# Kernel tuning notes

Hardware: AMD Instinct MI355X
Metric: run time of the kernel (lower is better)

## Reference

```python
import jax, jax.numpy as jnp
import numpy as np

V = 50000      # word vocab
CV = 128       # char vocab
E = 64         # char embedding size
H = 512        # GRU hidden / word embedding size
T = 20         # max spelling length
B = 2048       # batch of words


def setup_inputs() -> dict:
    key = jax.random.key(0)
    ks = jax.random.split(key, 8)
    chars = jax.random.randint(ks[0], (V, T), 1, CV)
    lengths = jax.random.randint(ks[1], (V,), 1, T + 1)
    mask = jnp.arange(T)[None, :] < lengths[:, None]
    chars = jnp.where(mask, chars, 0)  # padding_idx = 0 beyond each length
    spelling_table = jnp.concatenate([chars, lengths[:, None]], axis=1).astype(jnp.int32)
    data = jax.random.randint(ks[2], (B,), 0, V).astype(jnp.int32)
    s = 1.0 / np.sqrt(H)
    emb = (jax.random.normal(ks[3], (CV, E), jnp.float32) * 0.1).at[0].set(0.0)
    W_ih = jax.random.uniform(ks[4], (3 * H, E), jnp.float32, -s, s)
    W_hh = jax.random.uniform(ks[5], (3 * H, H), jnp.float32, -s, s)
    b_ih = jax.random.uniform(ks[6], (3 * H,), jnp.float32, -s, s)
    b_hh = jax.random.uniform(ks[7], (3 * H,), jnp.float32, -s, s)
    return {"data": data, "spelling_table": spelling_table, "emb": emb,
            "W_ih": W_ih, "W_hh": W_hh, "b_ih": b_ih, "b_hh": b_hh}


def reference(data, spelling_table, emb, W_ih, W_hh, b_ih, b_hh):
    H_ = W_hh.shape[1]
    rec = spelling_table[data]            # [B, T+1] gather of spellings
    spelling = rec[:, :-1]                # [B, T] char ids
    lengths = rec[:, -1]                  # [B]
    # torch.sort(lengths, descending=True): stable descending argsort
    perm = jnp.argsort(-lengths)
    sorted_sp = spelling[perm]            # [B, T]
    sorted_len = lengths[perm]            # [B]
    x = emb[sorted_sp]                    # [B, T, E]
    # precompute input projections for all timesteps (fused r|z|n gates)
    xW = jnp.einsum('bte,ge->btg', x, W_ih) + b_ih   # [B, T, 3H]
    valid = (jnp.arange(x.shape[1])[None, :] < sorted_len[:, None])  # [B, T]

    def step(h, inp):
        xw_t, v_t = inp                   # [B, 3H], [B, 1]
        hW = h @ W_hh.T + b_hh            # [B, 3H]
        xr, xz, xn = jnp.split(xw_t, 3, axis=-1)
        hr, hz, hn = jnp.split(hW, 3, axis=-1)
        r = jax.nn.sigmoid(xr + hr)
        z = jax.nn.sigmoid(xz + hz)
        n = jnp.tanh(xn + r * hn)
        h_new = (1.0 - z) * n + z * h
        h = jnp.where(v_t, h_new, h)      # packed-sequence semantics
        return h, None

    h0 = jnp.zeros((x.shape[0], H_), x.dtype)
    ht, _ = jax.lax.scan(step, h0, (jnp.swapaxes(xW, 0, 1), valid.T[:, :, None]))
    # faithful reproduction of the original's unsort: ht[sorted_length_idx]
    return ht[perm]
```

## Files before the change

kernel.cpp:

```cpp
#include <hip/hip_runtime.h>
#include <hip/hip_bf16.h>
#include <math.h>

#define B_  2048
#define E_  64
#define H_  512
#define T_  20

typedef _Float16 half8 __attribute__((ext_vector_type(8)));
typedef __attribute__((ext_vector_type(4))) float f32x4;
typedef unsigned long long u64;

#define mf16(a, b, c) __builtin_amdgcn_mfma_f32_16x16x32_f16(a, b, c, 0, 0, 0)

__device__ __forceinline__ float sigmoidf_(float x) {
  return 1.0f / (1.0f + __expf(-x));
}
__device__ __forceinline__ float tanh_fast(float x) {
  float e = __expf(2.0f * x);
  return 1.0f - 2.0f / (e + 1.0f);
}

__global__ __launch_bounds__(256) void k_setup(const int* __restrict__ data,
                                               const int* __restrict__ st,
                                               int* __restrict__ perm,
                                               int* __restrict__ iperm,
                                               int* __restrict__ Mt,
                                               int* __restrict__ bar) {
  __shared__ int lens[B_];
  __shared__ int hist[256][22];
  __shared__ int sub[16][22];
  __shared__ int subpre[16][22];
  __shared__ int cnt[32];
  __shared__ int offs[32];
  int tid = threadIdx.x;

  #pragma unroll
  for (int i = 0; i < 4; ++i) bar[tid * 4 + i] = 0;

  #pragma unroll
  for (int q = 0; q < 8; ++q) {
    int i = tid * 8 + q;
    lens[i] = st[data[i] * (T_ + 1) + T_];
  }
  #pragma unroll
  for (int L = 0; L < 22; ++L) hist[tid][L] = 0;
  #pragma unroll
  for (int q = 0; q < 8; ++q) hist[tid][lens[tid * 8 + q]]++;
  __syncthreads();

  for (int q = tid; q < 16 * 21; q += 256) {
    int g = q / 21, L = q % 21;
    int run = 0;
    for (int j = 0; j < 16; ++j) {
      int v = hist[g * 16 + j][L];
      hist[g * 16 + j][L] = run;
      run += v;
    }
    sub[g][L] = run;
  }
  __syncthreads();
  if (tid < 21) {
    int run = 0;
    for (int g = 0; g < 16; ++g) { subpre[g][tid] = run; run += sub[g][tid]; }
    cnt[tid] = run;
  }
  __syncthreads();
  if (tid <= 20) {
    int s = 0;
    for (int L = tid + 1; L <= 20; ++L) s += cnt[L];
    offs[tid] = s;
  }
  __syncthreads();
  if (tid < T_) Mt[tid] = offs[tid];

  int g = tid >> 4;
  #pragma unroll
  for (int q = 0; q < 8; ++q) {
    int i = tid * 8 + q;
    int L = lens[i];
    int rk = subpre[g][L] + hist[tid][L];
    hist[tid][L] += 1;
    perm[offs[L] + rk] = i;
  }
  __syncthreads();
  #pragma unroll
  for (int q = 0; q < 8; ++q) {
    int i = tid * 8 + q;
    iperm[perm[i]] = i;
  }
}

__global__ void k_schars(const int* __restrict__ data, const int* __restrict__ st,
                         const int* __restrict__ perm, int* __restrict__ schars_T) {
  int idx = blockIdx.x * 256 + threadIdx.x;
  if (idx >= B_ * T_) return;
  int t = idx >> 11;
  int j = idx & (B_ - 1);
  schars_T[idx] = st[data[perm[j]] * (T_ + 1) + t];
}

__global__ void k_wconv(const float* __restrict__ W_ih, const float* __restrict__ W_hh,
                        _Float16* __restrict__ Wp) {
  int idx = blockIdx.x * 256 + threadIdx.x;
  if (idx >= 8 * 18 * 12 * 512) return;
  int e = idx & 7;
  int l = (idx >> 3) & 63;
  int rest = idx >> 9;
  int g = rest % 3;  rest /= 3;
  int w = rest & 3;  rest >>= 2;
  int c = rest % 18;
  int cb = rest / 18;
  int grow = g * H_ + cb * 64 + w * 16 + (l & 15);
  int k = c * 32 + (l >> 4) * 8 + e;
  float v = (k < E_) ? W_ih[grow * E_ + k] : W_hh[grow * H_ + (k - E_)];
  Wp[idx] = (_Float16)v;
}

__global__ void k_embconv(const float* __restrict__ emb, _Float16* __restrict__ embp) {
  int idx = blockIdx.x * 256 + threadIdx.x;
  if (idx >= 128 * E_) return;
  embp[idx] = (_Float16)emb[idx];
}

__global__ __launch_bounds__(256, 1) void k_gru(
    const int* __restrict__ Mt, const int* __restrict__ schars_T,
    const _Float16* __restrict__ embp, const _Float16* __restrict__ Wp,
    const float* __restrict__ b_ih, const float* __restrict__ b_hh,
    _Float16* __restrict__ hq0, _Float16* __restrict__ hq1,
    const int* __restrict__ iperm, float* __restrict__ out,
    int* __restrict__ bar) {
  __shared__ __attribute__((aligned(16))) _Float16 As[64][512];
  __shared__ __attribute__((aligned(16))) _Float16 Hs[64][68];

  int bid = blockIdx.x;
  int rb = bid & 31, cb = bid >> 5;
  int m0 = rb * 64;
  int tid = threadIdx.x;
  int w = tid >> 6;
  int l = tid & 63;
  int ln = l & 15, kc = l >> 4;

  half8 wfr[54];
  const _Float16* wsrc = Wp + ((size_t)(cb * 18) * 12 + w * 3) * 512 + l * 8;
  #pragma unroll
  for (int c = 0; c < 18; ++c) {
    #pragma unroll
    for (int g = 0; g < 3; ++g)
      wfr[c * 3 + g] = *(const half8*)(wsrc + (c * 12 + g) * 512);
  }

  int colg = cb * 64 + w * 16 + ln;
  float br  = b_ih[colg] + b_hh[colg];
  float bz  = b_ih[H_ + colg] + b_hh[H_ + colg];
  float bnx = b_ih[2 * H_ + colg];
  float bnh = b_hh[2 * H_ + colg];

  float hreg[4][4];
  #pragma unroll
  for (int i = 0; i < 4; ++i)
    #pragma unroll
    for (int j = 0; j < 4; ++j) hreg[i][j] = 0.0f;

  int* barp = bar + rb * 32;

  for (int t = 0; t < T_; ++t) {
    int M = Mt[t];
    if (m0 >= M) break;
    const _Float16* hin = (t & 1) ? hq1 : hq0;
    _Float16*       hout = (t & 1) ? hq0 : hq1;

    int ch[4];
    #pragma unroll
    for (int rf = 0; rf < 4; ++rf)
      ch[rf] = schars_T[t * B_ + m0 + rf * 16 + ln];

    u64 sb[16][2];
    if (t > 0) {
      if (tid == 0) {
        int target = 8 * t;
        while (__hip_atomic_load(barp, __ATOMIC_RELAXED, __HIP_MEMORY_SCOPE_AGENT) < target) {}
      }
      __syncthreads();
      #pragma unroll
      for (int i = 0; i < 16; ++i) {
        int r = w * 16 + i;
        u64* src = (u64*)(hin + (size_t)(m0 + r) * H_) + ((l ^ (i & 7)) << 1);
        sb[i][0] = __hip_atomic_load(src, __ATOMIC_RELAXED, __HIP_MEMORY_SCOPE_AGENT);
        sb[i][1] = __hip_atomic_load(src + 1, __ATOMIC_RELAXED, __HIP_MEMORY_SCOPE_AGENT);
      }
    }

    f32x4 accr[4], accz[4], accnx[4], accnh[4];
    #pragma unroll
    for (int i = 0; i < 4; ++i) {
      accr[i] = (f32x4){0.f, 0.f, 0.f, 0.f};
      accz[i] = (f32x4){0.f, 0.f, 0.f, 0.f};
      accnx[i] = (f32x4){0.f, 0.f, 0.f, 0.f};
      accnh[i] = (f32x4){0.f, 0.f, 0.f, 0.f};
    }

    #pragma unroll
    for (int rf = 0; rf < 4; ++rf) {
      const _Float16* ep = embp + ch[rf] * E_ + kc * 8;
      half8 a0 = *(const half8*)ep;
      half8 a1 = *(const half8*)(ep + 32);
      accr[rf]  = mf16(a0, wfr[0], accr[rf]);
      accz[rf]  = mf16(a0, wfr[1], accz[rf]);
      accnx[rf] = mf16(a0, wfr[2], accnx[rf]);
      accr[rf]  = mf16(a1, wfr[3], accr[rf]);
      accz[rf]  = mf16(a1, wfr[4], accz[rf]);
      accnx[rf] = mf16(a1, wfr[5], accnx[rf]);
    }

    if (t > 0) {
      #pragma unroll
      for (int i = 0; i < 16; ++i) {
        int r = w * 16 + i;
        u64* dp = (u64*)&As[r][l * 8];
        dp[0] = sb[i][0];
        dp[1] = sb[i][1];
      }
    }
    __syncthreads();

    if (t > 0) {
      const _Float16* asb = &As[0][0];
      #pragma unroll
      for (int chk = 0; chk < 16; ++chk) {
        #pragma unroll
        for (int rf = 0; rf < 4; ++rf) {
          int r = rf * 16 + ln;
          half8 af = *(const half8*)(asb + r * 512 + (((chk * 4 + kc) ^ (ln & 7)) << 3));
          accr[rf]  = mf16(af, wfr[(chk + 2) * 3 + 0], accr[rf]);
          accz[rf]  = mf16(af, wfr[(chk + 2) * 3 + 1], accz[rf]);
          accnh[rf] = mf16(af, wfr[(chk + 2) * 3 + 2], accnh[rf]);
        }
      }
    }

    #pragma unroll
    for (int rf = 0; rf < 4; ++rf) {
      #pragma unroll
      for (int q = 0; q < 4; ++q) {
        int row_l = rf * 16 + kc * 4 + q;
        if (m0 + row_l < M) {
          float r_ = sigmoidf_(accr[rf][q] + br);
          float z_ = sigmoidf_(accz[rf][q] + bz);
          float n_ = tanh_fast(accnx[rf][q] + bnx + r_ * (accnh[rf][q] + bnh));
          float hnew = (1.0f - z_) * n_ + z_ * hreg[rf][q];
          hreg[rf][q] = hnew;
          Hs[row_l][w * 16 + ln] = (_Float16)hnew;
        }
      }
    }
    __syncthreads();

    #pragma unroll
    for (int j = 0; j < 4; ++j) {
      int c = tid + 256 * j;
      int row_l = c >> 4;
      int coff = (c & 15) * 4;
      if (m0 + row_l < M) {
        u64 v = *(const u64*)&Hs[row_l][coff];
        __hip_atomic_store((u64*)(hout + (size_t)(m0 + row_l) * H_ + cb * 64 + coff),
                           v, __ATOMIC_RELAXED, __HIP_MEMORY_SCOPE_AGENT);
      }
    }
    asm volatile("s_waitcnt vmcnt(0)" ::: "memory");
    __syncthreads();
    if (tid == 0) {
      __hip_atomic_fetch_add(barp, 1, __ATOMIC_RELAXED, __HIP_MEMORY_SCOPE_AGENT);
    }
  }

  #pragma unroll
  for (int rf = 0; rf < 4; ++rf) {
    #pragma unroll
    for (int q = 0; q < 4; ++q) {
      int row = m0 + rf * 16 + kc * 4 + q;
      out[(size_t)iperm[row] * H_ + colg] = hreg[rf][q];
    }
  }
}

extern "C" void kernel_launch(void* const* d_in, const int* in_sizes, int n_in,
                              void* d_out, int out_size, void* d_ws, size_t ws_size,
                              hipStream_t stream) {
  const int*   data = (const int*)d_in[0];
  const int*   st   = (const int*)d_in[1];
  const float* emb  = (const float*)d_in[2];
  const float* W_ih = (const float*)d_in[3];
  const float* W_hh = (const float*)d_in[4];
  const float* b_ih = (const float*)d_in[5];
  const float* b_hh = (const float*)d_in[6];
  float* out = (float*)d_out;

  _Float16* hq0  = (_Float16*)d_ws;
  _Float16* hq1  = hq0 + B_ * H_;
  _Float16* Wp   = hq1 + B_ * H_;
  _Float16* embp = Wp + 8 * 18 * 12 * 512;
  int* perm   = (int*)(embp + 128 * E_);
  int* iperm  = perm + B_;
  int* Mt     = iperm + B_;
  int* bar    = Mt + 32;
  int* schars = bar + 32 * 32;

  k_setup<<<1, 256, 0, stream>>>(data, st, perm, iperm, Mt, bar);
  k_schars<<<(B_ * T_ + 255) / 256, 256, 0, stream>>>(data, st, perm, schars);
  k_wconv<<<(8 * 18 * 12 * 512 + 255) / 256, 256, 0, stream>>>(W_ih, W_hh, Wp);
  k_embconv<<<(128 * E_ + 255) / 256, 256, 0, stream>>>(emb, embp);

  k_gru<<<dim3(256), dim3(256), 0, stream>>>(Mt, schars, embp, Wp, b_ih, b_hh,
                                             hq0, hq1, iperm, out, bar);
}
```

Baseline: 188.7 us.

## Replace row-group counter barrier with per-block flags and overlap own-slice MFMA

Each block now publishes a per-block step flag instead of incrementing a shared row-group counter. It also keeps its own hidden-state slice in shared memory and runs that slice's MFMAs before waiting on peers. Peer slices are then fetched and consumed chunk by chunk with a rotated order, so recurrence work overlaps the cross-block synchronisation and global loads. This adds all-thread polling of seven flags and more __syncthreads per step, and it relies on relaxed atomics for correctness.

```diff
diff --git a/kernel.cpp b/kernel.cpp
--- a/kernel.cpp
+++ b/kernel.cpp
@@ -73,6 +73,7 @@
   }
   __syncthreads();
   if (tid < T_) Mt[tid] = offs[tid];
+  if (tid >= T_ && tid < 32) Mt[tid] = 0;
 
   int g = tid >> 4;
   #pragma unroll
@@ -129,26 +130,36 @@
     const float* __restrict__ b_ih, const float* __restrict__ b_hh,
     _Float16* __restrict__ hq0, _Float16* __restrict__ hq1,
     const int* __restrict__ iperm, float* __restrict__ out,
-    int* __restrict__ bar) {
+    int* __restrict__ flags) {
   __shared__ __attribute__((aligned(16))) _Float16 As[64][512];
-  __shared__ __attribute__((aligned(16))) _Float16 Hs[64][68];
 
   int bid = blockIdx.x;
   int rb = bid & 31, cb = bid >> 5;
   int m0 = rb * 64;
   int tid = threadIdx.x;
-  int w = tid >> 6;
-  int l = tid & 63;
+  int w = tid >> 6, l = tid & 63;
   int ln = l & 15, kc = l >> 4;
+  int rS = tid >> 2, qS = tid & 3;
 
   half8 wfr[54];
-  const _Float16* wsrc = Wp + ((size_t)(cb * 18) * 12 + w * 3) * 512 + l * 8;
-  #pragma unroll
-  for (int c = 0; c < 18; ++c) {
-    #pragma unroll
-    for (int g = 0; g < 3; ++g)
-      wfr[c * 3 + g] = *(const half8*)(wsrc + (c * 12 + g) * 512);
-  }
+#define WLD(c, g) (*(const half8*)(Wp + ((((size_t)cb * 18 + (c)) * 4 + w) * 3 + (g)) * 512 + l * 8))
+  #pragma unroll
+  for (int g = 0; g < 3; ++g) {
+    wfr[0 + g] = WLD(0, g);
+    wfr[3 + g] = WLD(1, g);
+    wfr[6 + g] = WLD(2 + 2 * cb, g);
+    wfr[9 + g] = WLD(3 + 2 * cb, g);
+  }
+  #pragma unroll
+  for (int jj = 0; jj < 7; ++jj) {
+    int j = (cb + 1 + jj) & 7;
+    #pragma unroll
+    for (int c2 = 0; c2 < 2; ++c2)
+      #pragma unroll
+      for (int g = 0; g < 3; ++g)
+        wfr[12 + jj * 6 + c2 * 3 + g] = WLD(2 + 2 * j + c2, g);
+  }
+#undef WLD
 
   int colg = cb * 64 + w * 16 + ln;
   float br  = b_ih[colg] + b_hh[colg];
@@ -162,34 +173,21 @@
     #pragma unroll
     for (int j = 0; j < 4; ++j) hreg[i][j] = 0.0f;
 
-  int* barp = bar + rb * 32;
-
+  int myflag = rb * 8 + cb;
+  int Mnext = Mt[0];
+
+  #pragma unroll 1
   for (int t = 0; t < T_; ++t) {
-    int M = Mt[t];
+    int M = Mnext;
     if (m0 >= M) break;
-    const _Float16* hin = (t & 1) ? hq1 : hq0;
+    Mnext = Mt[t + 1];
+    const _Float16* hin  = (t & 1) ? hq1 : hq0;
     _Float16*       hout = (t & 1) ? hq0 : hq1;
 
     int ch[4];
     #pragma unroll
     for (int rf = 0; rf < 4; ++rf)
       ch[rf] = schars_T[t * B_ + m0 + rf * 16 + ln];
-
-    u64 sb[16][2];
-    if (t > 0) {
-      if (tid == 0) {
-        int target = 8 * t;
-        while (__hip_atomic_load(barp, __ATOMIC_RELAXED, __HIP_MEMORY_SCOPE_AGENT) < target) {}
-      }
-      __syncthreads();
-      #pragma unroll
-      for (int i = 0; i < 16; ++i) {
-        int r = w * 16 + i;
-        u64* src = (u64*)(hin + (size_t)(m0 + r) * H_) + ((l ^ (i & 7)) << 1);
-        sb[i][0] = __hip_atomic_load(src, __ATOMIC_RELAXED, __HIP_MEMORY_SCOPE_AGENT);
-        sb[i][1] = __hip_atomic_load(src + 1, __ATOMIC_RELAXED, __HIP_MEMORY_SCOPE_AGENT);
-      }
-    }
 
     f32x4 accr[4], accz[4], accnx[4], accnh[4];
     #pragma unroll
@@ -215,27 +213,62 @@
 
     if (t > 0) {
       #pragma unroll
-      for (int i = 0; i < 16; ++i) {
-        int r = w * 16 + i;
-        u64* dp = (u64*)&As[r][l * 8];
-        dp[0] = sb[i][0];
-        dp[1] = sb[i][1];
-      }
-    }
-    __syncthreads();
-
-    if (t > 0) {
-      const _Float16* asb = &As[0][0];
-      #pragma unroll
-      for (int chk = 0; chk < 16; ++chk) {
+      for (int c2 = 0; c2 < 2; ++c2)
         #pragma unroll
         for (int rf = 0; rf < 4; ++rf) {
           int r = rf * 16 + ln;
-          half8 af = *(const half8*)(asb + r * 512 + (((chk * 4 + kc) ^ (ln & 7)) << 3));
-          accr[rf]  = mf16(af, wfr[(chk + 2) * 3 + 0], accr[rf]);
-          accz[rf]  = mf16(af, wfr[(chk + 2) * 3 + 1], accz[rf]);
-          accnh[rf] = mf16(af, wfr[(chk + 2) * 3 + 2], accnh[rf]);
+          int slot = (c2 * 4 + kc) ^ (ln & 7);
+          half8 af = *(const half8*)((const char*)As + r * 1024 + cb * 128 + slot * 16);
+          accr[rf]  = mf16(af, wfr[6 + c2 * 3 + 0], accr[rf]);
+          accz[rf]  = mf16(af, wfr[6 + c2 * 3 + 1], accz[rf]);
+          accnh[rf] = mf16(af, wfr[6 + c2 * 3 + 2], accnh[rf]);
         }
+
+      int* fb = flags + rb * 8;
+      int ready = 0;
+      while (!ready) {
+        int acc = 1;
+        #pragma unroll
+        for (int jj = 0; jj < 7; ++jj) {
+          int j = (cb + 1 + jj) & 7;
+          int f = __hip_atomic_load(fb + j, __ATOMIC_RELAXED, __HIP_MEMORY_SCOPE_AGENT);
+          acc &= (f >= t) ? 1 : 0;
+        }
+        ready = acc;
+      }
+
+      u64 sb[7][4];
+      #pragma unroll
+      for (int jj = 0; jj < 7; ++jj) {
+        int j = (cb + 1 + jj) & 7;
+        const u64* gp = (const u64*)(hin + (size_t)(m0 + rS) * H_ + j * 64);
+        #pragma unroll
+        for (int i = 0; i < 4; ++i)
+          sb[jj][i] = __hip_atomic_load((u64*)(gp + qS + 4 * i),
+                                        __ATOMIC_RELAXED, __HIP_MEMORY_SCOPE_AGENT);
+      }
+
+      #pragma unroll
+      for (int jj = 0; jj < 7; ++jj) {
+        int j = (cb + 1 + jj) & 7;
+        #pragma unroll
+        for (int i = 0; i < 4; ++i) {
+          int u = qS + 4 * i;
+          int slot = (u >> 1) ^ (rS & 7);
+          *(u64*)((char*)As + rS * 1024 + j * 128 + slot * 16 + (u & 1) * 8) = sb[jj][i];
+        }
+        __syncthreads();
+        #pragma unroll
+        for (int c2 = 0; c2 < 2; ++c2)
+          #pragma unroll
+          for (int rf = 0; rf < 4; ++rf) {
+            int r = rf * 16 + ln;
+            int slot = (c2 * 4 + kc) ^ (ln & 7);
+            half8 af = *(const half8*)((const char*)As + r * 1024 + j * 128 + slot * 16);
+            accr[rf]  = mf16(af, wfr[12 + jj * 6 + c2 * 3 + 0], accr[rf]);
+            accz[rf]  = mf16(af, wfr[12 + jj * 6 + c2 * 3 + 1], accz[rf]);
+            accnh[rf] = mf16(af, wfr[12 + jj * 6 + c2 * 3 + 2], accnh[rf]);
+          }
       }
     }
 
@@ -248,30 +281,28 @@
           float r_ = sigmoidf_(accr[rf][q] + br);
           float z_ = sigmoidf_(accz[rf][q] + bz);
           float n_ = tanh_fast(accnx[rf][q] + bnx + r_ * (accnh[rf][q] + bnh));
-          float hnew = (1.0f - z_) * n_ + z_ * hreg[rf][q];
-          hreg[rf][q] = hnew;
-          Hs[row_l][w * 16 + ln] = (_Float16)hnew;
+          hreg[rf][q] = (1.0f - z_) * n_ + z_ * hreg[rf][q];
         }
+        int c = w * 16 + ln;
+        int slot = (c >> 3) ^ (row_l & 7);
+        *(_Float16*)((char*)As + row_l * 1024 + cb * 128 + slot * 16 + (c & 7) * 2) =
+            (_Float16)hreg[rf][q];
       }
     }
     __syncthreads();
 
     #pragma unroll
-    for (int j = 0; j < 4; ++j) {
-      int c = tid + 256 * j;
-      int row_l = c >> 4;
-      int coff = (c & 15) * 4;
-      if (m0 + row_l < M) {
-        u64 v = *(const u64*)&Hs[row_l][coff];
-        __hip_atomic_store((u64*)(hout + (size_t)(m0 + row_l) * H_ + cb * 64 + coff),
-                           v, __ATOMIC_RELAXED, __HIP_MEMORY_SCOPE_AGENT);
-      }
+    for (int i = 0; i < 4; ++i) {
+      int u = qS + 4 * i;
+      int slot = (u >> 1) ^ (rS & 7);
+      u64 v = *(const u64*)((const char*)As + rS * 1024 + cb * 128 + slot * 16 + (u & 1) * 8);
+      __hip_atomic_store((u64*)(hout + (size_t)(m0 + rS) * H_ + cb * 64) + u, v,
+                         __ATOMIC_RELAXED, __HIP_MEMORY_SCOPE_AGENT);
     }
     asm volatile("s_waitcnt vmcnt(0)" ::: "memory");
     __syncthreads();
-    if (tid == 0) {
-      __hip_atomic_fetch_add(barp, 1, __ATOMIC_RELAXED, __HIP_MEMORY_SCOPE_AGENT);
-    }
+    if (tid == 0)
+      __hip_atomic_store(flags + myflag, t + 1, __ATOMIC_RELAXED, __HIP_MEMORY_SCOPE_AGENT);
   }
 
   #pragma unroll
```

Measured after the change: 191.7 us. Within noise of the previous version (+1.6%).

## Precompute char-embedding input projections table and stream W_hh fragments from global

Applied to the files above, without the earlier changes.

Replaces the per-step input-projection MFMAs with a precomputed 128x1536 fp32 table (emb·W_ih^T plus biases), looked up per row by character id in the gate epilogue. W_hh weight fragments are no longer held in 54 registers. They are reloaded from global/L2 each timestep in double-buffered groups of 4 chunks, interleaved with the MFMA chunks. The intent is to free registers and drop the input GEMM. The cost is extra global traffic per step for weights and scattered table lookups in the epilogue.

```diff
diff --git a/kernel.cpp b/kernel.cpp
--- a/kernel.cpp
+++ b/kernel.cpp
@@ -26,7 +26,7 @@
                                                int* __restrict__ perm,
                                                int* __restrict__ iperm,
                                                int* __restrict__ Mt,
-                                               int* __restrict__ bar) {
+                                               int* __restrict__ flags) {
   __shared__ int lens[B_];
   __shared__ int hist[256][22];
   __shared__ int sub[16][22];
@@ -36,7 +36,7 @@
   int tid = threadIdx.x;
 
   #pragma unroll
-  for (int i = 0; i < 4; ++i) bar[tid * 4 + i] = 0;
+  for (int i = 0; i < 4; ++i) flags[tid * 4 + i] = 0;
 
   #pragma unroll
   for (int q = 0; q < 8; ++q) {
@@ -73,6 +73,7 @@
   }
   __syncthreads();
   if (tid < T_) Mt[tid] = offs[tid];
+  if (tid >= T_ && tid < 32) Mt[tid] = 0;
 
   int g = tid >> 4;
   #pragma unroll
@@ -100,33 +101,44 @@
   schars_T[idx] = st[data[perm[j]] * (T_ + 1) + t];
 }
 
-__global__ void k_wconv(const float* __restrict__ W_ih, const float* __restrict__ W_hh,
-                        _Float16* __restrict__ Wp) {
+__global__ void k_wconv(const float* __restrict__ W_hh, _Float16* __restrict__ Wp) {
   int idx = blockIdx.x * 256 + threadIdx.x;
-  if (idx >= 8 * 18 * 12 * 512) return;
+  if (idx >= 8 * 16 * 12 * 512) return;
   int e = idx & 7;
   int l = (idx >> 3) & 63;
   int rest = idx >> 9;
   int g = rest % 3;  rest /= 3;
-  int w = rest & 3;  rest >>= 2;
-  int c = rest % 18;
-  int cb = rest / 18;
-  int grow = g * H_ + cb * 64 + w * 16 + (l & 15);
+  int wc = rest & 3; rest >>= 2;
+  int c = rest % 16;
+  int cb = rest / 16;
+  int grow = g * H_ + cb * 64 + wc * 16 + (l & 15);
   int k = c * 32 + (l >> 4) * 8 + e;
-  float v = (k < E_) ? W_ih[grow * E_ + k] : W_hh[grow * H_ + (k - E_)];
-  Wp[idx] = (_Float16)v;
-}
-
-__global__ void k_embconv(const float* __restrict__ emb, _Float16* __restrict__ embp) {
-  int idx = blockIdx.x * 256 + threadIdx.x;
-  if (idx >= 128 * E_) return;
-  embp[idx] = (_Float16)emb[idx];
+  Wp[idx] = (_Float16)W_hh[grow * H_ + k];
+}
+
+__global__ __launch_bounds__(256) void k_embw(const float* __restrict__ emb,
+                                              const float* __restrict__ W_ih,
+                                              const float* __restrict__ b_ih,
+                                              const float* __restrict__ b_hh,
+                                              float* __restrict__ embW) {
+  int c = blockIdx.x;
+  int tid = threadIdx.x;
+  __shared__ float ev[64];
+  if (tid < 64) ev[tid] = emb[c * E_ + tid];
+  __syncthreads();
+  for (int o = tid; o < 3 * H_; o += 256) {
+    float s = b_ih[o];
+    if (o < 2 * H_) s += b_hh[o];
+    #pragma unroll
+    for (int k = 0; k < E_; ++k) s = fmaf(ev[k], W_ih[o * E_ + k], s);
+    embW[(size_t)c * (3 * H_) + o] = s;
+  }
 }
 
 __global__ __launch_bounds__(256, 1) void k_gru(
     const int* __restrict__ Mt, const int* __restrict__ schars_T,
-    const _Float16* __restrict__ embp, const _Float16* __restrict__ Wp,
-    const float* __restrict__ b_ih, const float* __restrict__ b_hh,
+    const float* __restrict__ embW, const _Float16* __restrict__ Wp,
+    const float* __restrict__ b_hh,
     _Float16* __restrict__ hq0, _Float16* __restrict__ hq1,
     const int* __restrict__ iperm, float* __restrict__ out,
     int* __restrict__ bar) {
@@ -141,19 +153,7 @@
   int l = tid & 63;
   int ln = l & 15, kc = l >> 4;
 
-  half8 wfr[54];
-  const _Float16* wsrc = Wp + ((size_t)(cb * 18) * 12 + w * 3) * 512 + l * 8;
-  #pragma unroll
-  for (int c = 0; c < 18; ++c) {
-    #pragma unroll
-    for (int g = 0; g < 3; ++g)
-      wfr[c * 3 + g] = *(const half8*)(wsrc + (c * 12 + g) * 512);
-  }
-
   int colg = cb * 64 + w * 16 + ln;
-  float br  = b_ih[colg] + b_hh[colg];
-  float bz  = b_ih[H_ + colg] + b_hh[H_ + colg];
-  float bnx = b_ih[2 * H_ + colg];
   float bnh = b_hh[2 * H_ + colg];
 
   float hreg[4][4];
@@ -163,6 +163,22 @@
     for (int j = 0; j < 4; ++j) hreg[i][j] = 0.0f;
 
   int* barp = bar + rb * 32;
+
+#define WLOAD(c, g) (*(const half8*)(Wp + \
+    (((size_t)(cb * 16 + (c)) * 4 + w) * 3 + (g)) * 512 + l * 8))
+
+#define H_CHUNK(c, F, FB)                                                      \
+  {                                                                            \
+    _Pragma("unroll")                                                          \
+    for (int rf = 0; rf < 4; ++rf) {                                           \
+      int r = rf * 16 + ln;                                                    \
+      half8 af = *(const half8*)((const _Float16*)As + r * 512 +               \
+                                 ((((c) * 4 + kc) ^ (ln & 7)) << 3));          \
+      accr[rf]  = mf16(af, F[((c) - (FB)) * 3 + 0], accr[rf]);                 \
+      accz[rf]  = mf16(af, F[((c) - (FB)) * 3 + 1], accz[rf]);                 \
+      accnh[rf] = mf16(af, F[((c) - (FB)) * 3 + 2], accnh[rf]);                \
+    }                                                                          \
+  }
 
   for (int t = 0; t < T_; ++t) {
     int M = Mt[t];
@@ -170,18 +186,28 @@
     const _Float16* hin = (t & 1) ? hq1 : hq0;
     _Float16*       hout = (t & 1) ? hq0 : hq1;
 
-    int ch[4];
+    int chv[4][4];
     #pragma unroll
     for (int rf = 0; rf < 4; ++rf)
-      ch[rf] = schars_T[t * B_ + m0 + rf * 16 + ln];
-
-    u64 sb[16][2];
+      #pragma unroll
+      for (int q = 0; q < 4; ++q)
+        chv[rf][q] = schars_T[t * B_ + m0 + rf * 16 + kc * 4 + q];
+
+    f32x4 accr[4], accz[4], accnh[4];
+    #pragma unroll
+    for (int i = 0; i < 4; ++i) {
+      accr[i] = (f32x4){0.f, 0.f, 0.f, 0.f};
+      accz[i] = (f32x4){0.f, 0.f, 0.f, 0.f};
+      accnh[i] = (f32x4){0.f, 0.f, 0.f, 0.f};
+    }
+
     if (t > 0) {
       if (tid == 0) {
         int target = 8 * t;
         while (__hip_atomic_load(barp, __ATOMIC_RELAXED, __HIP_MEMORY_SCOPE_AGENT) < target) {}
       }
       __syncthreads();
+      u64 sb[16][2];
       #pragma unroll
       for (int i = 0; i < 16; ++i) {
         int r = w * 16 + i;
@@ -189,31 +215,16 @@
         sb[i][0] = __hip_atomic_load(src, __ATOMIC_RELAXED, __HIP_MEMORY_SCOPE_AGENT);
         sb[i][1] = __hip_atomic_load(src + 1, __ATOMIC_RELAXED, __HIP_MEMORY_SCOPE_AGENT);
       }
-    }
-
-    f32x4 accr[4], accz[4], accnx[4], accnh[4];
-    #pragma unroll
-    for (int i = 0; i < 4; ++i) {
-      accr[i] = (f32x4){0.f, 0.f, 0.f, 0.f};
-      accz[i] = (f32x4){0.f, 0.f, 0.f, 0.f};
-      accnx[i] = (f32x4){0.f, 0.f, 0.f, 0.f};
-      accnh[i] = (f32x4){0.f, 0.f, 0.f, 0.f};
-    }
-
-    #pragma unroll
-    for (int rf = 0; rf < 4; ++rf) {
-      const _Float16* ep = embp + ch[rf] * E_ + kc * 8;
-      half8 a0 = *(const half8*)ep;
-      half8 a1 = *(const half8*)(ep + 32);
-      accr[rf]  = mf16(a0, wfr[0], accr[rf]);
-      accz[rf]  = mf16(a0, wfr[1], accz[rf]);
-      accnx[rf] = mf16(a0, wfr[2], accnx[rf]);
-      accr[rf]  = mf16(a1, wfr[3], accr[rf]);
-      accz[rf]  = mf16(a1, wfr[4], accz[rf]);
-      accnx[rf] = mf16(a1, wfr[5], accnx[rf]);
-    }
-
-    if (t > 0) {
+
+      half8 wfA[12], wfB[12];
+      #pragma unroll
+      for (int cc = 0; cc < 4; ++cc)
+        #pragma unroll
+        for (int g = 0; g < 3; ++g) {
+          wfA[cc * 3 + g] = WLOAD(cc, g);
+          wfB[cc * 3 + g] = WLOAD(4 + cc, g);
+        }
+
       #pragma unroll
       for (int i = 0; i < 16; ++i) {
         int r = w * 16 + i;
@@ -221,22 +232,27 @@
         dp[0] = sb[i][0];
         dp[1] = sb[i][1];
       }
-    }
-    __syncthreads();
-
-    if (t > 0) {
-      const _Float16* asb = &As[0][0];
-      #pragma unroll
-      for (int chk = 0; chk < 16; ++chk) {
+      __syncthreads();
+
+      H_CHUNK(0, wfA, 0) H_CHUNK(1, wfA, 0) H_CHUNK(2, wfA, 0) H_CHUNK(3, wfA, 0)
+      __builtin_amdgcn_sched_barrier(0);
+      #pragma unroll
+      for (int cc = 0; cc < 4; ++cc)
         #pragma unroll
-        for (int rf = 0; rf < 4; ++rf) {
-          int r = rf * 16 + ln;
-          half8 af = *(const half8*)(asb + r * 512 + (((chk * 4 + kc) ^ (ln & 7)) << 3));
-          accr[rf]  = mf16(af, wfr[(chk + 2) * 3 + 0], accr[rf]);
-          accz[rf]  = mf16(af, wfr[(chk + 2) * 3 + 1], accz[rf]);
-          accnh[rf] = mf16(af, wfr[(chk + 2) * 3 + 2], accnh[rf]);
-        }
-      }
+        for (int g = 0; g < 3; ++g)
+          wfA[cc * 3 + g] = WLOAD(8 + cc, g);
+      H_CHUNK(4, wfB, 4) H_CHUNK(5, wfB, 4) H_CHUNK(6, wfB, 4) H_CHUNK(7, wfB, 4)
+      __builtin_amdgcn_sched_barrier(0);
+      #pragma unroll
+      for (int cc = 0; cc < 4; ++cc)
+        #pragma unroll
+        for (int g = 0; g < 3; ++g)
+          wfB[cc * 3 + g] = WLOAD(12 + cc, g);
+      H_CHUNK(8, wfA, 8) H_CHUNK(9, wfA, 8) H_CHUNK(10, wfA, 8) H_CHUNK(11, wfA, 8)
+      __builtin_amdgcn_sched_barrier(0);
+      H_CHUNK(12, wfB, 12) H_CHUNK(13, wfB, 12) H_CHUNK(14, wfB, 12) H_CHUNK(15, wfB, 12)
+    } else {
+      __syncthreads();
     }
 
     #pragma unroll
@@ -245,9 +261,10 @@
       for (int q = 0; q < 4; ++q) {
         int row_l = rf * 16 + kc * 4 + q;
         if (m0 + row_l < M) {
-          float r_ = sigmoidf_(accr[rf][q] + br);
-          float z_ = sigmoidf_(accz[rf][q] + bz);
-          float n_ = tanh_fast(accnx[rf][q] + bnx + r_ * (accnh[rf][q] + bnh));
+          const float* ew = embW + (size_t)chv[rf][q] * (3 * H_) + colg;
+          float r_ = sigmoidf_(accr[rf][q] + ew[0]);
+          float z_ = sigmoidf_(accz[rf][q] + ew[H_]);
+          float n_ = tanh_fast(ew[2 * H_] + r_ * (accnh[rf][q] + bnh));
           float hnew = (1.0f - z_) * n_ + z_ * hreg[rf][q];
           hreg[rf][q] = hnew;
           Hs[row_l][w * 16 + ln] = (_Float16)hnew;
@@ -269,10 +286,11 @@
     }
     asm volatile("s_waitcnt vmcnt(0)" ::: "memory");
     __syncthreads();
-    if (tid == 0) {
+    if (tid == 0)
       __hip_atomic_fetch_add(barp, 1, __ATOMIC_RELAXED, __HIP_MEMORY_SCOPE_AGENT);
-    }
-  }
+  }
+#undef H_CHUNK
+#undef WLOAD
 
   #pragma unroll
   for (int rf = 0; rf < 4; ++rf) {
@@ -299,18 +317,18 @@
   _Float16* hq0  = (_Float16*)d_ws;
   _Float16* hq1  = hq0 + B_ * H_;
   _Float16* Wp   = hq1 + B_ * H_;
-  _Float16* embp = Wp + 8 * 18 * 12 * 512;
-  int* perm   = (int*)(embp + 128 * E_);
+  float*    embW = (float*)(Wp + 8 * 16 * 12 * 512);
+  int* perm   = (int*)(embW + 128 * 3 * H_);
   int* iperm  = perm + B_;
   int* Mt     = iperm + B_;
-  int* bar    = Mt + 32;
-  int* schars = bar + 32 * 32;
-
-  k_setup<<<1, 256, 0, stream>>>(data, st, perm, iperm, Mt, bar);
+  int* flags  = Mt + 32;
+  int* schars = flags + 1024;
+
+  k_setup<<<1, 256, 0, stream>>>(data, st, perm, iperm, Mt, flags);
   k_schars<<<(B_ * T_ + 255) / 256, 256, 0, stream>>>(data, st, perm, schars);
-  k_wconv<<<(8 * 18 * 12 * 512 + 255) / 256, 256, 0, stream>>>(W_ih, W_hh, Wp);
-  k_embconv<<<(128 * E_ + 255) / 256, 256, 0, stream>>>(emb, embp);
-
-  k_gru<<<dim3(256), dim3(256), 0, stream>>>(Mt, schars, embp, Wp, b_ih, b_hh,
-                                             hq0, hq1, iperm, out, bar);
-}
+  k_wconv<<<(8 * 16 * 12 * 512 + 255) / 256, 256, 0, stream>>>(W_hh, Wp);
+  k_embw<<<128, 256, 0, stream>>>(emb, W_ih, b_ih, b_hh, embW);
+
+  k_gru<<<dim3(256), dim3(256), 0, stream>>>(Mt, schars, embW, Wp, b_hh,
+                                             hq0, hq1, iperm, out, flags);
+}
```

Result: slower. 229.9 us (+21.8%).
